# Optimization experiments

Measured on AMD Instinct MI355X. Metric: run time of the kernel, lower is better.

The kernel has to match this reference:

```python
import jax, jax.numpy as jnp
from jax import lax
import numpy as np

S = 2        # scale_factor
K = 5        # upsample_kernel_size
M = 64       # m_channels
C_IN = 128

def setup_inputs() -> dict:
    key = jax.random.key(0)
    k1, k2, k3, k4, k5 = jax.random.split(key, 5)
    B, C, H, W = 8, C_IN, 64, 64
    x = jax.random.normal(k1, (B, C, H, W), dtype=jnp.float32)
    compress_w = jax.random.normal(k2, (M, C, 1, 1), dtype=jnp.float32) * 0.05
    compress_b = jax.random.normal(k3, (M,), dtype=jnp.float32) * 0.05
    n_out = K * K * S * S  # 100
    encoder_w = jax.random.normal(k4, (n_out, M, 3, 3), dtype=jnp.float32) * 0.05
    encoder_b = jax.random.normal(k5, (n_out,), dtype=jnp.float32) * 0.05
    return {"x": x, "compress_w": compress_w, "compress_b": compress_b,
            "encoder_w": encoder_w, "encoder_b": encoder_b}

def _carafe(x, compress_w, compress_b, encoder_w, encoder_b):
    B, C, H, W = x.shape
    k, s = K, S
    nH, nW = s * H, s * W
    # 1x1 compress conv
    m = jnp.einsum('bchw,mc->bmhw', x, compress_w[:, :, 0, 0]) + compress_b[None, :, None, None]
    # 3x3 encoder conv, stride 1, pad 1 (SAME)
    ker = lax.conv_general_dilated(m, encoder_w, window_strides=(1, 1), padding='SAME',
                                   dimension_numbers=('NCHW', 'OIHW', 'NCHW'))
    ker = ker + encoder_b[None, :, None, None]  # (B, k*k*s*s, H, W)
    # PixelShuffle(s): (B, k*k, s, s, H, W) -> (B, k*k, H, s, W, s) -> (B, k*k, nH, nW)
    ker = ker.reshape(B, k * k, s, s, H, W).transpose(0, 1, 4, 2, 5, 3).reshape(B, k * k, nH, nW)
    ker = jax.nn.softmax(ker, axis=1)
    # Unfold(k, stride=1, pad=k//2): stack k*k shifted views, ordering (kh outer, kw inner)
    pad = k // 2
    xp = jnp.pad(x, ((0, 0), (0, 0), (pad, pad), (pad, pad)))
    patches = jnp.stack([xp[:, :, i:i + H, j:j + W] for i in range(k) for j in range(k)],
                        axis=2)  # (B, C, k*k, H, W)
    # nearest upsample by s on spatial dims
    up = jnp.repeat(jnp.repeat(patches, s, axis=3), s, axis=4)  # (B, C, k*k, nH, nW)
    # weighted local sum
    out = jnp.sum(up * ker[:, None, :, :, :], axis=2)  # (B, C, nH, nW)
    return out

def reference(x, compress_w, compress_b, encoder_w, encoder_b):
    return _carafe(x, compress_w, compress_b, encoder_w, encoder_b)
```

## Files before the change

kernel.cpp:

```cpp
#include <hip/hip_runtime.h>
#include <math.h>


typedef __attribute__((ext_vector_type(8))) short short8;
typedef __attribute__((ext_vector_type(4))) float floatx4;
typedef __attribute__((ext_vector_type(2))) float v2f;

__device__ __forceinline__ unsigned short f2bf(float f) {
  union { float f; unsigned int u; } v; v.f = f;
  unsigned int u = v.u + 0x7fffu + ((v.u >> 16) & 1u);
  return (unsigned short)(u >> 16);
}
__device__ __forceinline__ void unpack2(unsigned int u, float& lo, float& hi) {
  union { unsigned int u; float f; } a, b;
  a.u = u << 16; b.u = u & 0xffff0000u;
  lo = a.f; hi = b.f;
}
__device__ __forceinline__ v2f unpack2v(unsigned int u) {
  union { unsigned int u; float f; } a, b;
  a.u = u << 16; b.u = u & 0xffff0000u;
  return (v2f){a.f, b.f};
}

__global__ __launch_bounds__(256) void k_prep(
    const float* __restrict__ ew, const float* __restrict__ cw,
    unsigned short* __restrict__ a_prep, float* __restrict__ cwT,
    unsigned short* __restrict__ xpad) {
  const int blk = blockIdx.x;
  if (blk < 320) {
    int idx = blk * 256 + (int)threadIdx.x;
    if (idx < 9 * 128 * 64) {
      int mo = idx & 63;
      int n = (idx >> 6) & 127;
      int tap = idx >> 13;
      float v = (n < 100) ? ew[(n * 64 + mo) * 9 + tap] : 0.f;
      a_prep[idx] = f2bf(v);
    } else {
      int r = idx - 9 * 128 * 64;
      int c = r >> 6, mo = r & 63;
      cwT[c * 64 + mo] = cw[mo * 128 + c];
    }
  } else {
    int local = blk - 320;
    for (int i = threadIdx.x; i < 800; i += 256) {
      int which = (i >= 400);
      int k = i - which * 400;
      unsigned int* pd =
          (unsigned int*)(xpad + (size_t)(local * 2 + which) * 4896);
      int u32idx;
      if (k < 72) {
        u32idx = k;
      } else if (k < 144) {
        u32idx = 2376 + (k - 72);
      } else {
        int j = k - 144;
        int r = 2 + (j >> 2), s = j & 3;
        u32idx = r * 36 + (s ? 32 + s : 0);
      }
      pd[u32idx] = 0u;
    }
  }
}

__global__ __launch_bounds__(256) void k_comp_pad(
    const float* __restrict__ x, const float* __restrict__ cwT,
    const float* __restrict__ cb, unsigned short* __restrict__ m_t,
    unsigned short* __restrict__ xpad) {
  __shared__ __align__(16) float xs[128 * 64];
  const int lb = (((int)blockIdx.x & 7) << 6) | ((int)blockIdx.x >> 3);
  const int b = lb >> 6;
  const int h = lb & 63;
  const int t = (int)threadIdx.x;

  const float* xrow = x + (((size_t)b * 128) * 64 + h) * 64;
  unsigned short* xpd = xpad + (size_t)b * 128 * 4896 + (h + 2) * 72 + 2;
#pragma unroll
  for (int it = 0; it < 32; ++it) {
    int idx = it * 256 + t;
    int c = idx >> 6, w = idx & 63;
    float v = xrow[(size_t)c * 4096 + w];
    xs[idx] = v;
    xpd[(size_t)c * 4896 + w] = f2bf(v);
  }
  __syncthreads();

  const int wv = __builtin_amdgcn_readfirstlane(t >> 6);
  const int lane = t & 63;
  const int mo0 = wv * 16;

  float acc[16];
#pragma unroll
  for (int k = 0; k < 16; ++k) acc[k] = 0.f;

  const float* wp = cwT + mo0;

#pragma unroll 4
  for (int c = 0; c < 128; ++c) {
    float xv = xs[c * 64 + lane];
#pragma unroll
    for (int k = 0; k < 16; ++k)
      acc[k] = fmaf(xv, wp[c * 64 + k], acc[k]);
  }

#pragma unroll
  for (int k = 0; k < 16; ++k) acc[k] += cb[mo0 + k];

  __syncthreads();
  unsigned short* ms = (unsigned short*)xs;
#pragma unroll
  for (int k = 0; k < 8; ++k) {
    unsigned int p = ((unsigned int)f2bf(acc[2 * k + 1]) << 16) | f2bf(acc[2 * k]);
    *(unsigned int*)&ms[lane * 72 + mo0 + 2 * k] = p;
  }
  __syncthreads();
#pragma unroll
  for (int rep = 0; rep < 2; ++rep) {
    int idx = t + rep * 256;
    uint4 v = *(const uint4*)&ms[(idx >> 3) * 72 + (idx & 7) * 8];
    *(uint4*)&m_t[(size_t)lb * 4096 + idx * 8] = v;
  }
}

__global__ __launch_bounds__(256) void k_main(
    const unsigned short* __restrict__ m_t, const unsigned short* __restrict__ a_prep,
    const float* __restrict__ eb, const unsigned short* __restrict__ xpad,
    float* __restrict__ out) {
  __shared__ __align__(16) float raw[128 * 66];
  unsigned short* m_s = (unsigned short*)raw;
  unsigned short* wgt_s = (unsigned short*)raw;
  const int lb = (((int)blockIdx.x & 7) << 6) | ((int)blockIdx.x >> 3);
  const int b = lb >> 6;
  const int h = lb & 63;
  const int t = (int)threadIdx.x;

  for (int idx = t; idx < 3 * 64 * 8; idx += 256) {
    int r = idx >> 9;
    int rem = idx & 511;
    int w = rem >> 3, u = rem & 7;
    int hh = h + r - 1;
    uint4 val = make_uint4(0u, 0u, 0u, 0u);
    if (hh >= 0 && hh < 64)
      val = *(const uint4*)&m_t[(((b * 64 + hh) * 64 + w) * 64) + u * 8];
    *(uint4*)&m_s[(r * 64 + w) * 72 + u * 8] = val;
  }
  __syncthreads();

  const int wave = t >> 6, lane = t & 63;
  const int quad = lane >> 4, col = lane & 15;
  const int nbase = wave * 32;

  const floatx4 z4 = {0.f, 0.f, 0.f, 0.f};
  floatx4 acc[2][4];
#pragma unroll
  for (int i = 0; i < 2; ++i)
#pragma unroll
    for (int p = 0; p < 4; ++p) acc[i][p] = z4;

  const short8 z8 = {0, 0, 0, 0, 0, 0, 0, 0};

#pragma unroll
  for (int tap = 0; tap < 9; ++tap) {
    const int dh = tap / 3, dw = tap % 3;
#pragma unroll
    for (int half = 0; half < 2; ++half) {
      const int mo0 = half * 32;
      short8 a0 = *(const short8*)&a_prep[((tap * 128 + nbase + col) * 64) + mo0 + quad * 8];
      short8 a1 = *(const short8*)&a_prep[((tap * 128 + nbase + 16 + col) * 64) + mo0 + quad * 8];
#pragma unroll
      for (int p = 0; p < 4; ++p) {
        int wsrc = p * 16 + col + dw - 1;
        int wc = min(max(wsrc, 0), 63);
        short8 bf = *(const short8*)&m_s[(dh * 64 + wc) * 72 + mo0 + quad * 8];
        if (wsrc < 0 || wsrc > 63) bf = z8;
        acc[0][p] = __builtin_amdgcn_mfma_f32_16x16x32_bf16(a0, bf, acc[0][p], 0, 0, 0);
        acc[1][p] = __builtin_amdgcn_mfma_f32_16x16x32_bf16(a1, bf, acc[1][p], 0, 0, 0);
      }
    }
  }

  __syncthreads();
#pragma unroll
  for (int i = 0; i < 2; ++i)
#pragma unroll
    for (int p = 0; p < 4; ++p)
#pragma unroll
      for (int r = 0; r < 4; ++r)
        raw[(nbase + i * 16 + quad * 4 + r) * 66 + p * 16 + col] = acc[i][p][r];
  __syncthreads();

  const int q = wave;
  float v[25];
  float mx = -1e30f;
#pragma unroll
  for (int kk = 0; kk < 25; ++kk) {
    v[kk] = raw[(kk * 4 + q) * 66 + lane] + eb[kk * 4 + q];
    mx = fmaxf(mx, v[kk]);
  }
  float s = 0.f;
#pragma unroll
  for (int kk = 0; kk < 25; ++kk) {
    v[kk] = __expf(v[kk] - mx);
    s += v[kk];
  }
  float inv = 1.f / s;

  __syncthreads();
  {
    const int ohl = q >> 1;
    const int owp = 2 * lane + (q & 1);
#pragma unroll
    for (int kk = 0; kk < 25; ++kk)
      wgt_s[(ohl * 25 + kk) * 128 + owp] = f2bf(v[kk] * inv);
  }
  __syncthreads();

  const int wg = t & 15;
  const int cg = t >> 4;
  const int w0 = wg * 4;

  for (int chalf = 0; chalf < 2; ++chalf) {
    const int c0 = chalf * 64 + cg * 4;
    const unsigned short* xb =
        xpad + ((size_t)(b * 128 + c0) * 4896) + h * 72 + w0;

    v2f accB[2][4][4];
#pragma unroll
    for (int oh = 0; oh < 2; ++oh)
#pragma unroll
      for (int ch = 0; ch < 4; ++ch)
#pragma unroll
        for (int k = 0; k < 4; ++k) accB[oh][ch][k] = (v2f){0.f, 0.f};

    for (int i = 0; i < 5; ++i) {
      float xr[4][8];
#pragma unroll
      for (int ch = 0; ch < 4; ++ch) {
        uint4 rawv = *(const uint4*)(xb + ch * 4896 + i * 72);
        unpack2(rawv.x, xr[ch][0], xr[ch][1]);
        unpack2(rawv.y, xr[ch][2], xr[ch][3]);
        unpack2(rawv.z, xr[ch][4], xr[ch][5]);
        unpack2(rawv.w, xr[ch][6], xr[ch][7]);
      }
#pragma unroll
      for (int j = 0; j < 5; ++j) {
        const int ij = i * 5 + j;
#pragma unroll
        for (int oh = 0; oh < 2; ++oh) {
          uint4 wr = *(const uint4*)&wgt_s[(oh * 25 + ij) * 128 + w0 * 2];
          v2f wp[4];
          wp[0] = unpack2v(wr.x);
          wp[1] = unpack2v(wr.y);
          wp[2] = unpack2v(wr.z);
          wp[3] = unpack2v(wr.w);
#pragma unroll
          for (int k = 0; k < 4; ++k)
#pragma unroll
            for (int ch = 0; ch < 4; ++ch) {
              float xv = xr[ch][k + j];
              v2f xvv = {xv, xv};
              accB[oh][ch][k] += xvv * wp[k];
            }
        }
      }
    }

#pragma unroll
    for (int ch = 0; ch < 4; ++ch)
#pragma unroll
      for (int oh = 0; oh < 2; ++oh) {
        float* orow =
            out + ((size_t)(b * 128 + c0 + ch) * 128 + (2 * h + oh)) * 128 + w0 * 2;
        float4 f0 = make_float4(accB[oh][ch][0].x, accB[oh][ch][0].y,
                                accB[oh][ch][1].x, accB[oh][ch][1].y);
        float4 f1 = make_float4(accB[oh][ch][2].x, accB[oh][ch][2].y,
                                accB[oh][ch][3].x, accB[oh][ch][3].y);
        *(float4*)orow = f0;
        *(float4*)(orow + 4) = f1;
      }
  }
}

extern "C" void kernel_launch(void* const* d_in, const int* in_sizes, int n_in,
                              void* d_out, int out_size, void* d_ws, size_t ws_size,
                              hipStream_t stream) {
  (void)in_sizes; (void)n_in; (void)out_size; (void)ws_size;
  const float* x  = (const float*)d_in[0];
  const float* cw = (const float*)d_in[1];
  const float* cb = (const float*)d_in[2];
  const float* ew = (const float*)d_in[3];
  const float* eb = (const float*)d_in[4];
  float* out = (float*)d_out;

  char* wsb = (char*)d_ws;
  unsigned short* m_t    = (unsigned short*)(wsb);
  unsigned short* a_prep = (unsigned short*)(wsb + 4194304);
  unsigned short* xpad   = (unsigned short*)(wsb + 4341760);
  float*          cwT    = (float*)(wsb + 14368768);

  k_prep<<<dim3(832), dim3(256), 0, stream>>>(ew, cw, a_prep, cwT, xpad);
  k_comp_pad<<<dim3(512), dim3(256), 0, stream>>>(x, cwT, cb, m_t, xpad);
  k_main<<<dim3(512), dim3(256), 0, stream>>>(m_t, a_prep, eb, xpad, out);
}
```

Baseline: 134.7 us.

## Double k_main block size to 512 threads and redistribute work across waves

k_main now launches 512 threads per block. In the encoder GEMM each wave computes one 16-row output tile instead of two, and in the reassembly stage each thread handles all 128 channels' worth of work split by output row rather than by channel half. Only the first four waves run the softmax. The aim is more waves per CU and less per-thread register pressure (accumulator arrays halved) to hide latency, at the cost of idle waves during softmax and more threads competing for the same LDS.

```diff
diff --git a/kernel.cpp b/kernel.cpp
--- a/kernel.cpp
+++ b/kernel.cpp
@@ -121,7 +121,7 @@
   }
 }
 
-__global__ __launch_bounds__(256) void k_main(
+__global__ __launch_bounds__(512, 4) void k_main(
     const unsigned short* __restrict__ m_t, const unsigned short* __restrict__ a_prep,
     const float* __restrict__ eb, const unsigned short* __restrict__ xpad,
     float* __restrict__ out) {
@@ -133,7 +133,7 @@
   const int h = lb & 63;
   const int t = (int)threadIdx.x;
 
-  for (int idx = t; idx < 3 * 64 * 8; idx += 256) {
+  for (int idx = t; idx < 3 * 64 * 8; idx += 512) {
     int r = idx >> 9;
     int rem = idx & 511;
     int w = rem >> 3, u = rem & 7;
@@ -147,14 +147,12 @@
 
   const int wave = t >> 6, lane = t & 63;
   const int quad = lane >> 4, col = lane & 15;
-  const int nbase = wave * 32;
+  const int nbase = wave * 16;
 
   const floatx4 z4 = {0.f, 0.f, 0.f, 0.f};
-  floatx4 acc[2][4];
-#pragma unroll
-  for (int i = 0; i < 2; ++i)
-#pragma unroll
-    for (int p = 0; p < 4; ++p) acc[i][p] = z4;
+  floatx4 acc[4];
+#pragma unroll
+  for (int p = 0; p < 4; ++p) acc[p] = z4;
 
   const short8 z8 = {0, 0, 0, 0, 0, 0, 0, 0};
 
@@ -165,47 +163,46 @@
     for (int half = 0; half < 2; ++half) {
       const int mo0 = half * 32;
       short8 a0 = *(const short8*)&a_prep[((tap * 128 + nbase + col) * 64) + mo0 + quad * 8];
-      short8 a1 = *(const short8*)&a_prep[((tap * 128 + nbase + 16 + col) * 64) + mo0 + quad * 8];
 #pragma unroll
       for (int p = 0; p < 4; ++p) {
         int wsrc = p * 16 + col + dw - 1;
         int wc = min(max(wsrc, 0), 63);
         short8 bf = *(const short8*)&m_s[(dh * 64 + wc) * 72 + mo0 + quad * 8];
         if (wsrc < 0 || wsrc > 63) bf = z8;
-        acc[0][p] = __builtin_amdgcn_mfma_f32_16x16x32_bf16(a0, bf, acc[0][p], 0, 0, 0);
-        acc[1][p] = __builtin_amdgcn_mfma_f32_16x16x32_bf16(a1, bf, acc[1][p], 0, 0, 0);
-      }
-    }
-  }
-
-  __syncthreads();
-#pragma unroll
-  for (int i = 0; i < 2; ++i)
-#pragma unroll
-    for (int p = 0; p < 4; ++p)
-#pragma unroll
-      for (int r = 0; r < 4; ++r)
-        raw[(nbase + i * 16 + quad * 4 + r) * 66 + p * 16 + col] = acc[i][p][r];
-  __syncthreads();
-
-  const int q = wave;
+        acc[p] = __builtin_amdgcn_mfma_f32_16x16x32_bf16(a0, bf, acc[p], 0, 0, 0);
+      }
+    }
+  }
+
+  __syncthreads();
+#pragma unroll
+  for (int p = 0; p < 4; ++p)
+#pragma unroll
+    for (int r = 0; r < 4; ++r)
+      raw[(nbase + quad * 4 + r) * 66 + p * 16 + col] = acc[p][r];
+  __syncthreads();
+
+  const int q = wave & 3;
   float v[25];
-  float mx = -1e30f;
-#pragma unroll
-  for (int kk = 0; kk < 25; ++kk) {
-    v[kk] = raw[(kk * 4 + q) * 66 + lane] + eb[kk * 4 + q];
-    mx = fmaxf(mx, v[kk]);
-  }
-  float s = 0.f;
-#pragma unroll
-  for (int kk = 0; kk < 25; ++kk) {
-    v[kk] = __expf(v[kk] - mx);
-    s += v[kk];
-  }
-  float inv = 1.f / s;
-
-  __syncthreads();
-  {
+  float inv = 0.f;
+  if (wave < 4) {
+    float mx = -1e30f;
+#pragma unroll
+    for (int kk = 0; kk < 25; ++kk) {
+      v[kk] = raw[(kk * 4 + q) * 66 + lane] + eb[kk * 4 + q];
+      mx = fmaxf(mx, v[kk]);
+    }
+    float s = 0.f;
+#pragma unroll
+    for (int kk = 0; kk < 25; ++kk) {
+      v[kk] = __expf(v[kk] - mx);
+      s += v[kk];
+    }
+    inv = 1.f / s;
+  }
+
+  __syncthreads();
+  if (wave < 4) {
     const int ohl = q >> 1;
     const int owp = 2 * lane + (q & 1);
 #pragma unroll
@@ -217,19 +214,16 @@
   const int wg = t & 15;
   const int cg = t >> 4;
   const int w0 = wg * 4;
-
-  for (int chalf = 0; chalf < 2; ++chalf) {
-    const int c0 = chalf * 64 + cg * 4;
-    const unsigned short* xb =
-        xpad + ((size_t)(b * 128 + c0) * 4896) + h * 72 + w0;
-
-    v2f accB[2][4][4];
-#pragma unroll
-    for (int oh = 0; oh < 2; ++oh)
-#pragma unroll
-      for (int ch = 0; ch < 4; ++ch)
-#pragma unroll
-        for (int k = 0; k < 4; ++k) accB[oh][ch][k] = (v2f){0.f, 0.f};
+  const int c0 = cg * 4;
+  const unsigned short* xb =
+      xpad + ((size_t)(b * 128 + c0) * 4896) + h * 72 + w0;
+
+  for (int oh = 0; oh < 2; ++oh) {
+    v2f accB[4][4];
+#pragma unroll
+    for (int ch = 0; ch < 4; ++ch)
+#pragma unroll
+      for (int k = 0; k < 4; ++k) accB[ch][k] = (v2f){0.f, 0.f};
 
     for (int i = 0; i < 5; ++i) {
       float xr[4][8];
@@ -244,39 +238,34 @@
 #pragma unroll
       for (int j = 0; j < 5; ++j) {
         const int ij = i * 5 + j;
-#pragma unroll
-        for (int oh = 0; oh < 2; ++oh) {
-          uint4 wr = *(const uint4*)&wgt_s[(oh * 25 + ij) * 128 + w0 * 2];
-          v2f wp[4];
-          wp[0] = unpack2v(wr.x);
-          wp[1] = unpack2v(wr.y);
-          wp[2] = unpack2v(wr.z);
-          wp[3] = unpack2v(wr.w);
-#pragma unroll
-          for (int k = 0; k < 4; ++k)
-#pragma unroll
-            for (int ch = 0; ch < 4; ++ch) {
-              float xv = xr[ch][k + j];
-              v2f xvv = {xv, xv};
-              accB[oh][ch][k] += xvv * wp[k];
-            }
-        }
-      }
-    }
-
-#pragma unroll
-    for (int ch = 0; ch < 4; ++ch)
-#pragma unroll
-      for (int oh = 0; oh < 2; ++oh) {
-        float* orow =
-            out + ((size_t)(b * 128 + c0 + ch) * 128 + (2 * h + oh)) * 128 + w0 * 2;
-        float4 f0 = make_float4(accB[oh][ch][0].x, accB[oh][ch][0].y,
-                                accB[oh][ch][1].x, accB[oh][ch][1].y);
-        float4 f1 = make_float4(accB[oh][ch][2].x, accB[oh][ch][2].y,
-                                accB[oh][ch][3].x, accB[oh][ch][3].y);
-        *(float4*)orow = f0;
-        *(float4*)(orow + 4) = f1;
-      }
+        uint4 wr = *(const uint4*)&wgt_s[(oh * 25 + ij) * 128 + w0 * 2];
+        v2f wp[4];
+        wp[0] = unpack2v(wr.x);
+        wp[1] = unpack2v(wr.y);
+        wp[2] = unpack2v(wr.z);
+        wp[3] = unpack2v(wr.w);
+#pragma unroll
+        for (int k = 0; k < 4; ++k)
+#pragma unroll
+          for (int ch = 0; ch < 4; ++ch) {
+            float xv = xr[ch][k + j];
+            v2f xvv = {xv, xv};
+            accB[ch][k] += xvv * wp[k];
+          }
+      }
+    }
+
+#pragma unroll
+    for (int ch = 0; ch < 4; ++ch) {
+      float* orow =
+          out + ((size_t)(b * 128 + c0 + ch) * 128 + (2 * h + oh)) * 128 + w0 * 2;
+      float4 f0 = make_float4(accB[ch][0].x, accB[ch][0].y,
+                              accB[ch][1].x, accB[ch][1].y);
+      float4 f1 = make_float4(accB[ch][2].x, accB[ch][2].y,
+                              accB[ch][3].x, accB[ch][3].y);
+      *(float4*)orow = f0;
+      *(float4*)(orow + 4) = f1;
+    }
   }
 }
 
@@ -299,5 +288,5 @@
 
   k_prep<<<dim3(832), dim3(256), 0, stream>>>(ew, cw, a_prep, cwT, xpad);
   k_comp_pad<<<dim3(512), dim3(256), 0, stream>>>(x, cwT, cb, m_t, xpad);
-  k_main<<<dim3(512), dim3(256), 0, stream>>>(m_t, a_prep, eb, xpad, out);
-}
+  k_main<<<dim3(512), dim3(512), 0, stream>>>(m_t, a_prep, eb, xpad, out);
+}
```

Measured after the change: 324.8 us. 141% more time.
